# Optimization experiments

Measured on AMD Instinct MI355X. Metric: run time of the kernel, lower is better.

The kernel has to match this reference:

```python
import jax, jax.numpy as jnp
import numpy as np

INPUT_SIZE = 512
N_THETA = 608  # backcast 512 + forecast 96
N_EXPERTS = 8
TOP_K = 2
LN_EPS = 1e-5


def setup_inputs() -> dict:
    key = jax.random.key(0)
    ks = jax.random.split(key, 5)
    B = 8192
    s = 0.02
    return {
        "insample_y": jax.random.normal(ks[0], (B, INPUT_SIZE), dtype=jnp.float32),
        "ln_gamma": jnp.ones((INPUT_SIZE,), dtype=jnp.float32),
        "ln_beta": jnp.zeros((INPUT_SIZE,), dtype=jnp.float32),
        "Wg": jax.random.normal(ks[1], (INPUT_SIZE, N_EXPERTS), dtype=jnp.float32) * s,
        "W0": jax.random.normal(ks[2], (N_EXPERTS, INPUT_SIZE, 512), dtype=jnp.float32) * s,
        "Wmid": jax.random.normal(ks[3], (3, N_EXPERTS, 512, 512), dtype=jnp.float32) * s,
        "Wout": jax.random.normal(ks[4], (N_EXPERTS, 512, N_THETA), dtype=jnp.float32) * s,
    }


def _layer_norm(x, gamma, beta):
    mu = jnp.mean(x, axis=-1, keepdims=True)
    var = jnp.mean(jnp.square(x - mu), axis=-1, keepdims=True)
    return (x - mu) * jax.lax.rsqrt(var + LN_EPS) * gamma + beta


def reference(insample_y, ln_gamma, ln_beta, Wg, W0, Wmid, Wout):
    x = insample_y  # [B, input_size]
    # Gate: LayerNorm -> Linear(no bias) -> top-k -> softmax over selected logits
    gate_logits = _layer_norm(x, ln_gamma, ln_beta) @ Wg            # [B, E]
    top_vals, top_idx = jax.lax.top_k(gate_logits, TOP_K)           # [B, k]
    gate_w = jax.nn.softmax(top_vals, axis=-1)                      # [B, k]

    # Experts (bias-free MLPs), evaluated densely for all experts
    z = jnp.einsum('bi,eih->beh', x, W0)                            # first linear, no activation
    for l in range(Wmid.shape[0]):
        z = jax.nn.relu(jnp.einsum('beh,eho->beo', z, Wmid[l]))
    theta_all = jnp.einsum('beh,eht->bet', z, Wout)                 # [B, E, n_theta]

    # Combine top-k expert outputs with gate weights
    theta_sel = jnp.take_along_axis(theta_all, top_idx[:, :, None], axis=1)  # [B, k, n_theta]
    theta = jnp.einsum('bk,bkt->bt', gate_w, theta_sel)             # [B, n_theta]

    # Identity basis: split theta into backcast / forecast
    backcast = theta[:, :INPUT_SIZE]
    forecast = theta[:, INPUT_SIZE:]
    return backcast, forecast
```

## Files before the change

### kernel.cpp

```cpp
#include <hip/hip_runtime.h>
#include <hip/hip_bf16.h>
#include <stdint.h>


#define B_ROWS 8192
#define I_DIM  512
#define H_DIM  512
#define E_NUM  8
#define T_DIM  608
#define T_PAD  640
#define CAP    2304
#define TPE    18
#define NT     144
#define NPAD   18432

typedef unsigned short ushort_t;
typedef __attribute__((ext_vector_type(8))) __bf16 bf16x8;
typedef __attribute__((ext_vector_type(8))) unsigned short ushort8;
typedef __attribute__((ext_vector_type(4))) float floatx4;

__device__ __forceinline__ void gload_lds16(const void* g, void* l) {
  __builtin_amdgcn_global_load_lds(
      (const __attribute__((address_space(1))) unsigned int*)g,
      (__attribute__((address_space(3))) unsigned int*)l, 16, 0, 0);
}

__device__ __forceinline__ ushort_t f2bf(float v) {
  __hip_bfloat16 h = __float2bfloat16(v);
  return __builtin_bit_cast(unsigned short, h);
}

__global__ __launch_bounds__(256) void gate_cast_k(
    const float* __restrict__ x, const float* __restrict__ gamma,
    const float* __restrict__ beta, const float* __restrict__ Wg,
    ushort_t* __restrict__ xb, int2* __restrict__ gidx, float2* __restrict__ gw)
{
  const int row  = (blockIdx.x * blockDim.x + threadIdx.x) >> 6;
  const int lane = threadIdx.x & 63;
  const float* xr = x + (size_t)row * I_DIM + lane * 8;
  float4 a = *(const float4*)(xr);
  float4 b = *(const float4*)(xr + 4);
  float xs[8] = {a.x, a.y, a.z, a.w, b.x, b.y, b.z, b.w};

  float s = 0.f;
#pragma unroll
  for (int j = 0; j < 8; ++j) s += xs[j];
#pragma unroll
  for (int off = 32; off; off >>= 1) s += __shfl_xor(s, off);
  const float mu = s * (1.0f / I_DIM);

  float vs = 0.f;
#pragma unroll
  for (int j = 0; j < 8; ++j) { float d = xs[j] - mu; vs += d * d; }
#pragma unroll
  for (int off = 32; off; off >>= 1) vs += __shfl_xor(vs, off);
  const float rstd = rsqrtf(vs * (1.0f / I_DIM) + 1e-5f);

  float lg[8] = {0.f, 0.f, 0.f, 0.f, 0.f, 0.f, 0.f, 0.f};
  const float* gmr = gamma + lane * 8;
  const float* btr = beta + lane * 8;
#pragma unroll
  for (int j = 0; j < 8; ++j) {
    const float y = (xs[j] - mu) * rstd * gmr[j] + btr[j];
    const float* wr = Wg + (size_t)(lane * 8 + j) * E_NUM;
#pragma unroll
    for (int e = 0; e < 8; ++e) lg[e] += y * wr[e];
  }
#pragma unroll
  for (int e = 0; e < 8; ++e)
#pragma unroll
    for (int off = 32; off; off >>= 1) lg[e] += __shfl_xor(lg[e], off);

  ushort8 o;
#pragma unroll
  for (int j = 0; j < 8; ++j) o[j] = f2bf(xs[j]);
  *(ushort8*)(xb + (size_t)row * I_DIM + lane * 8) = o;

  if (lane == 0) {
    int i0 = 0; float b0 = lg[0];
#pragma unroll
    for (int e = 1; e < 8; ++e) if (lg[e] > b0) { b0 = lg[e]; i0 = e; }
    int i1 = -1; float b1 = -3.4e38f;
#pragma unroll
    for (int e = 0; e < 8; ++e) if (e != i0 && lg[e] > b1) { b1 = lg[e]; i1 = e; }
    const float w0 = 1.0f / (1.0f + __expf(b1 - b0));
    gidx[row] = make_int2(i0, i1);
    gw[row] = make_float2(w0, 1.0f - w0);
  }
}

__global__ __launch_bounds__(256) void assign_k(
    const int2* __restrict__ gidx, const float2* __restrict__ gw,
    int* __restrict__ rowmap, float* __restrict__ wmap,
    int* __restrict__ cursor)
{
  __shared__ int lcnt[E_NUM];
  __shared__ int lbase[E_NUM];
  const int tid = threadIdx.x;
  const int row = blockIdx.x * 256 + tid;
  if (tid < E_NUM) lcnt[tid] = 0;
  __syncthreads();
  const int2 g = gidx[row];
  const float2 w = gw[row];
  const int r0 = atomicAdd(&lcnt[g.x], 1);
  const int r1 = atomicAdd(&lcnt[g.y], 1);
  __syncthreads();
  if (tid < E_NUM) lbase[tid] = atomicAdd(&cursor[tid], lcnt[tid]);
  __syncthreads();
  const int p0 = g.x * CAP + lbase[g.x] + r0;
  rowmap[p0] = row; wmap[p0] = w.x;
  const int p1 = g.y * CAP + lbase[g.y] + r1;
  rowmap[p1] = row; wmap[p1] = w.y;
}

__global__ __launch_bounds__(256) void transpose_cast_k(
    const float* __restrict__ src, ushort_t* __restrict__ dst,
    int R, int C, size_t srcBStr, size_t dstBStr)
{
  __shared__ float tile[32][33];
  src += (size_t)blockIdx.z * srcBStr;
  dst += (size_t)blockIdx.z * dstBStr;
  const int c0 = blockIdx.x * 32, r0 = blockIdx.y * 32;
  const int tx = threadIdx.x, ty = threadIdx.y;
#pragma unroll
  for (int i = 0; i < 4; ++i)
    tile[ty + i * 8][tx] = src[(size_t)(r0 + ty + i * 8) * C + c0 + tx];
  __syncthreads();
#pragma unroll
  for (int i = 0; i < 4; ++i) {
    const int c = c0 + ty + i * 8;
    if (c < C) dst[(size_t)c * R + r0 + tx] = f2bf(tile[tx][ty + i * 8]);
  }
}

template <bool GATHER, bool RELU, bool FINAL>
__global__ __launch_bounds__(256, 2) void gemm_k(
    const ushort_t* __restrict__ A,
    const ushort_t* __restrict__ B,
    size_t bEStr,
    const int* __restrict__ rowmap, const float* __restrict__ wmap,
    const int* __restrict__ cursor,
    ushort_t* __restrict__ Z,
    float* __restrict__ out)
{
  constexpr int K = 512;
  constexpr int BK = 64;
  constexpr int NSTEP = K / BK;
  __shared__ ushort_t lA[2][128 * BK];
  __shared__ ushort_t lB[2][128 * BK];
  __shared__ float wrow[128];
  __shared__ int rrow[128];

  const int t = blockIdx.x;
  const int e = t / TPE;
  if ((t - e * TPE) * 128 >= cursor[e]) return;
  const int zr0 = t * 128;
  const int bn0 = blockIdx.y * 128;

  const int tid = threadIdx.x, wid = tid >> 6, lane = tid & 63;
  const int rl = lane >> 3;
  const int kl = lane & 7;
  const int ks = (kl ^ rl) * 8;

  const ushort_t* Bb = B + (size_t)e * bEStr + (size_t)bn0 * K;
  const ushort_t* gA[4];
  const ushort_t* gB[4];
#pragma unroll
  for (int j = 0; j < 4; ++j) {
    const int rloc = wid * 32 + j * 8 + rl;
    int grow;
    if (GATHER) grow = rowmap[zr0 + rloc];
    else        grow = zr0 + rloc;
    gA[j] = A + (size_t)grow * K + ks;
    gB[j] = Bb + (size_t)rloc * K + ks;
  }

  auto stage = [&](int tt) {
    ushort_t* da = lA[tt & 1];
    ushort_t* db = lB[tt & 1];
    const int k0 = tt * BK;
#pragma unroll
    for (int j = 0; j < 4; ++j) {
      gload_lds16(gA[j] + k0, da + (wid * 32 + j * 8) * BK);
      gload_lds16(gB[j] + k0, db + (wid * 32 + j * 8) * BK);
    }
  };

  floatx4 acc[4][4] = {};
  const int wm = (wid >> 1) * 64, wn = (wid & 1) * 64;
  const int fr = lane & 15, q = lane >> 4;

  stage(0);
  asm volatile("s_waitcnt vmcnt(0)" ::: "memory");
  __builtin_amdgcn_s_barrier();

#pragma unroll
  for (int step = 0; step < NSTEP; ++step) {
    const int cur = step & 1;
    if (step < NSTEP - 1) stage(step + 1);

    bf16x8 af[4][2], bfr[4][2];
    const char* bA = (const char*)lA[cur];
    const char* bB = (const char*)lB[cur];
#pragma unroll
    for (int mi = 0; mi < 4; ++mi) {
      const int row = wm + mi * 16 + fr;
      const int rb = row * 128, rx = (row & 7) << 4;
#pragma unroll
      for (int kk = 0; kk < 2; ++kk)
        af[mi][kk] = *(const bf16x8*)(bA + ((rb + kk * 64 + q * 16) ^ rx));
    }
#pragma unroll
    for (int ni = 0; ni < 4; ++ni) {
      const int row = wn + ni * 16 + fr;
      const int rb = row * 128, rx = (row & 7) << 4;
#pragma unroll
      for (int kk = 0; kk < 2; ++kk)
        bfr[ni][kk] = *(const bf16x8*)(bB + ((rb + kk * 64 + q * 16) ^ rx));
    }
#pragma unroll
    for (int kk = 0; kk < 2; ++kk)
#pragma unroll
      for (int mi = 0; mi < 4; ++mi)
#pragma unroll
        for (int ni = 0; ni < 4; ++ni)
          acc[mi][ni] = __builtin_amdgcn_mfma_f32_16x16x32_bf16(
              af[mi][kk], bfr[ni][kk], acc[mi][ni], 0, 0, 0);

    if (step < NSTEP - 1) {
      asm volatile("s_waitcnt vmcnt(0)" ::: "memory");
      __builtin_amdgcn_s_barrier();
    }
  }

  if (!FINAL) {
    ushort_t* Zb = Z + (size_t)zr0 * H_DIM + bn0;
#pragma unroll
    for (int mi = 0; mi < 4; ++mi)
#pragma unroll
      for (int r = 0; r < 4; ++r) {
        const int row = wm + mi * 16 + q * 4 + r;
        ushort_t* zr = Zb + (size_t)row * H_DIM + wn + fr;
#pragma unroll
        for (int ni = 0; ni < 4; ++ni) {
          float v = acc[mi][ni][r];
          if (RELU) v = fmaxf(v, 0.0f);
          zr[ni * 16] = f2bf(v);
        }
      }
  } else {
    if (tid < 128) {
      wrow[tid] = wmap[zr0 + tid];
      rrow[tid] = rowmap[zr0 + tid];
    }
    __syncthreads();
#pragma unroll
    for (int mi = 0; mi < 4; ++mi)
#pragma unroll
      for (int r = 0; r < 4; ++r) {
        const int row = wm + mi * 16 + q * 4 + r;
        const float w = wrow[row];
        if (w != 0.0f) {
          const size_t orig = rrow[row];
#pragma unroll
          for (int ni = 0; ni < 4; ++ni) {
            const int col = bn0 + wn + ni * 16 + fr;
            if (col < T_DIM) {
              const float v = acc[mi][ni][r] * w;
              float* dst = (col < I_DIM)
                  ? out + orig * I_DIM + col
                  : out + (size_t)B_ROWS * I_DIM + orig * (T_DIM - I_DIM) +
                        (col - I_DIM);
              atomicAdd(dst, v);
            }
          }
        }
      }
  }
}

extern "C" void kernel_launch(void* const* d_in, const int* in_sizes, int n_in,
                              void* d_out, int out_size, void* d_ws,
                              size_t ws_size, hipStream_t stream) {
  const float* x     = (const float*)d_in[0];
  const float* gamma = (const float*)d_in[1];
  const float* beta  = (const float*)d_in[2];
  const float* Wg    = (const float*)d_in[3];
  const float* W0    = (const float*)d_in[4];
  const float* Wmid  = (const float*)d_in[5];
  const float* Wout  = (const float*)d_in[6];
  float* out = (float*)d_out;

  char* ws = (char*)d_ws;
  size_t off = 0;
  auto alloc = [&](size_t bytes) -> char* {
    char* p = ws + off;
    off += (bytes + 255) & ~(size_t)255;
    return p;
  };

  const size_t SQ = (size_t)H_DIM * H_DIM;
  ushort_t* xb    = (ushort_t*)alloc((size_t)B_ROWS * I_DIM * 2);
  ushort_t* W0t   = (ushort_t*)alloc((size_t)E_NUM * SQ * 2);
  ushort_t* Wmidt = (ushort_t*)alloc((size_t)3 * E_NUM * SQ * 2);
  ushort_t* Woutt = (ushort_t*)alloc((size_t)E_NUM * T_PAD * H_DIM * 2);
  int2*   gidx  = (int2*)alloc((size_t)B_ROWS * sizeof(int2));
  float2* gwv   = (float2*)alloc((size_t)B_ROWS * sizeof(float2));
  int*   rmap   = (int*)alloc(NPAD * sizeof(int));
  float* wmap   = (float*)alloc(NPAD * sizeof(float));
  int*   cursor = (int*)alloc(E_NUM * sizeof(int));
  ushort_t* z0 = (ushort_t*)alloc((size_t)NPAD * H_DIM * 2);
  ushort_t* z1 = (ushort_t*)alloc((size_t)NPAD * H_DIM * 2);

  hipMemsetAsync(d_out, 0, (size_t)out_size * sizeof(float), stream);
  hipMemsetAsync(rmap, 0, NPAD * sizeof(int), stream);
  hipMemsetAsync(wmap, 0, NPAD * sizeof(float), stream);
  hipMemsetAsync(cursor, 0, E_NUM * sizeof(int), stream);

  gate_cast_k<<<dim3(B_ROWS / 4), 256, 0, stream>>>(x, gamma, beta, Wg, xb,
                                                    gidx, gwv);
  transpose_cast_k<<<dim3(16, 16, 8), dim3(32, 8), 0, stream>>>(
      W0, W0t, 512, 512, SQ, SQ);
  transpose_cast_k<<<dim3(16, 16, 24), dim3(32, 8), 0, stream>>>(
      Wmid, Wmidt, 512, 512, SQ, SQ);
  transpose_cast_k<<<dim3(19, 16, 8), dim3(32, 8), 0, stream>>>(
      Wout, Woutt, 512, 608, (size_t)512 * 608, (size_t)T_PAD * 512);
  assign_k<<<dim3(B_ROWS / 256), 256, 0, stream>>>(gidx, gwv, rmap, wmap,
                                                   cursor);

  const dim3 gmid(NT, H_DIM / 128);
  const dim3 gfin(NT, T_PAD / 128);
  gemm_k<true, false, false><<<gmid, 256, 0, stream>>>(
      xb, W0t, SQ, rmap, wmap, cursor, z0, nullptr);
  gemm_k<false, true, false><<<gmid, 256, 0, stream>>>(
      z0, Wmidt + 0 * E_NUM * SQ, SQ, rmap, wmap, cursor, z1, nullptr);
  gemm_k<false, true, false><<<gmid, 256, 0, stream>>>(
      z1, Wmidt + 1 * E_NUM * SQ, SQ, rmap, wmap, cursor, z0, nullptr);
  gemm_k<false, true, false><<<gmid, 256, 0, stream>>>(
      z0, Wmidt + 2 * E_NUM * SQ, SQ, rmap, wmap, cursor, z1, nullptr);
  gemm_k<false, false, true><<<gfin, 256, 0, stream>>>(
      z1, Woutt, (size_t)T_PAD * H_DIM, rmap, wmap, cursor, nullptr, out);
}
```

Before: 277.4 us.

## Halve GEMM M-tile to 64 rows and interleave expert tiles across blocks

```diff
diff --git a/kernel.cpp b/kernel.cpp
--- a/kernel.cpp
+++ b/kernel.cpp
@@ -10,8 +10,8 @@
 #define T_DIM  608
 #define T_PAD  640
 #define CAP    2304
-#define TPE    18
-#define NT     144
+#define TPW    36
+#define MT     288
 #define NPAD   18432
 
 typedef unsigned short ushort_t;
@@ -134,7 +134,7 @@
 }
 
 template <bool GATHER, bool RELU, bool FINAL>
-__global__ __launch_bounds__(256, 2) void gemm_k(
+__global__ __launch_bounds__(256, 3) void gemm_k(
     const ushort_t* __restrict__ A,
     const ushort_t* __restrict__ B,
     size_t bEStr,
@@ -146,48 +146,53 @@
   constexpr int K = 512;
   constexpr int BK = 64;
   constexpr int NSTEP = K / BK;
-  __shared__ ushort_t lA[2][128 * BK];
-  __shared__ ushort_t lB[2][128 * BK];
-  __shared__ float wrow[128];
-  __shared__ int rrow[128];
+  __shared__ char lA[2][64 * 128];
+  __shared__ char lB[2][128 * 128];
+  __shared__ float wrow[64];
+  __shared__ int rrow[64];
 
   const int t = blockIdx.x;
-  const int e = t / TPE;
-  if ((t - e * TPE) * 128 >= cursor[e]) return;
-  const int zr0 = t * 128;
+  const int e = t & 7;
+  const int lt = t >> 3;
+  if (lt * 64 >= cursor[e]) return;
+  const int zr0 = e * CAP + lt * 64;
   const int bn0 = blockIdx.y * 128;
 
   const int tid = threadIdx.x, wid = tid >> 6, lane = tid & 63;
-  const int rl = lane >> 3;
-  const int kl = lane & 7;
-  const int ks = (kl ^ rl) * 8;
+  const int sr = tid >> 3;
+  const int sk = tid & 7;
 
   const ushort_t* Bb = B + (size_t)e * bEStr + (size_t)bn0 * K;
-  const ushort_t* gA[4];
+  const ushort_t* gA[2];
   const ushort_t* gB[4];
 #pragma unroll
-  for (int j = 0; j < 4; ++j) {
-    const int rloc = wid * 32 + j * 8 + rl;
+  for (int p = 0; p < 2; ++p) {
+    const int r = p * 32 + sr;
     int grow;
-    if (GATHER) grow = rowmap[zr0 + rloc];
-    else        grow = zr0 + rloc;
-    gA[j] = A + (size_t)grow * K + ks;
-    gB[j] = Bb + (size_t)rloc * K + ks;
+    if (GATHER) grow = rowmap[zr0 + r];
+    else        grow = zr0 + r;
+    gA[p] = A + (size_t)grow * K + ((sk ^ (r & 7)) * 8);
+  }
+#pragma unroll
+  for (int p = 0; p < 4; ++p) {
+    const int r = p * 32 + sr;
+    gB[p] = Bb + (size_t)r * K + ((sk ^ (r & 7)) * 8);
   }
 
   auto stage = [&](int tt) {
-    ushort_t* da = lA[tt & 1];
-    ushort_t* db = lB[tt & 1];
+    char* da = lA[tt & 1];
+    char* db = lB[tt & 1];
     const int k0 = tt * BK;
 #pragma unroll
-    for (int j = 0; j < 4; ++j) {
-      gload_lds16(gA[j] + k0, da + (wid * 32 + j * 8) * BK);
-      gload_lds16(gB[j] + k0, db + (wid * 32 + j * 8) * BK);
-    }
+    for (int p = 0; p < 2; ++p)
+      gload_lds16(gA[p] + k0, da + (p * 32 + sr) * 128 + sk * 16);
+#pragma unroll
+    for (int p = 0; p < 4; ++p)
+      gload_lds16(gB[p] + k0, db + (p * 32 + sr) * 128 + sk * 16);
   };
 
-  floatx4 acc[4][4] = {};
-  const int wm = (wid >> 1) * 64, wn = (wid & 1) * 64;
+  floatx4 acc[2][4] = {};
+  const int wm = (wid >> 1) * 32, wn = (wid & 1) * 64;
   const int fr = lane & 15, q = lane >> 4;
 
   stage(0);
@@ -199,11 +204,11 @@
     const int cur = step & 1;
     if (step < NSTEP - 1) stage(step + 1);
 
-    bf16x8 af[4][2], bfr[4][2];
-    const char* bA = (const char*)lA[cur];
-    const char* bB = (const char*)lB[cur];
-#pragma unroll
-    for (int mi = 0; mi < 4; ++mi) {
+    bf16x8 af[2][2], bfr[4][2];
+    const char* bA = lA[cur];
+    const char* bB = lB[cur];
+#pragma unroll
+    for (int mi = 0; mi < 2; ++mi) {
       const int row = wm + mi * 16 + fr;
       const int rb = row * 128, rx = (row & 7) << 4;
 #pragma unroll
@@ -221,7 +226,7 @@
 #pragma unroll
     for (int kk = 0; kk < 2; ++kk)
 #pragma unroll
-      for (int mi = 0; mi < 4; ++mi)
+      for (int mi = 0; mi < 2; ++mi)
 #pragma unroll
         for (int ni = 0; ni < 4; ++ni)
           acc[mi][ni] = __builtin_amdgcn_mfma_f32_16x16x32_bf16(
@@ -236,7 +241,7 @@
   if (!FINAL) {
     ushort_t* Zb = Z + (size_t)zr0 * H_DIM + bn0;
 #pragma unroll
-    for (int mi = 0; mi < 4; ++mi)
+    for (int mi = 0; mi < 2; ++mi)
 #pragma unroll
       for (int r = 0; r < 4; ++r) {
         const int row = wm + mi * 16 + q * 4 + r;
@@ -249,13 +254,13 @@
         }
       }
   } else {
-    if (tid < 128) {
+    if (tid < 64) {
       wrow[tid] = wmap[zr0 + tid];
       rrow[tid] = rowmap[zr0 + tid];
     }
     __syncthreads();
 #pragma unroll
-    for (int mi = 0; mi < 4; ++mi)
+    for (int mi = 0; mi < 2; ++mi)
 #pragma unroll
       for (int r = 0; r < 4; ++r) {
         const int row = wm + mi * 16 + q * 4 + r;
@@ -328,8 +333,8 @@
   assign_k<<<dim3(B_ROWS / 256), 256, 0, stream>>>(gidx, gwv, rmap, wmap,
                                                    cursor);
 
-  const dim3 gmid(NT, H_DIM / 128);
-  const dim3 gfin(NT, T_PAD / 128);
+  const dim3 gmid(MT, H_DIM / 128);
+  const dim3 gfin(MT, T_PAD / 128);
   gemm_k<true, false, false><<<gmid, 256, 0, stream>>>(
       xb, W0t, SQ, rmap, wmap, cursor, z0, nullptr);
   gemm_k<false, true, false><<<gmid, 256, 0, stream>>>(
```

After: 260.0 us. -6.3%, faster.
